# Performance work log

Measured on AMD Instinct MI355X. Metric: run time of the kernel, lower is better.

The kernel has to match this reference:

```python
import jax, jax.numpy as jnp
import numpy as np

# --- fixed physical constants (module params are requires_grad=False) ---
G = 9.81
M = 0.1667
CAF = 5.0 * 0.25 * M * G          # tanh(0) -> ratio = 1.0 exactly
CAR = CAF
LF = 0.09 - 0.036
LR = 0.036
IZ = 0.000267                      # tanh(0) -> pow_ratio = 0 -> Iz_base
THROTTLE_OFFSET = 0.24
THROTTLE_RATIO = 6.98
DT = 0.01
RES_BOUNDS = jnp.array([0.05 * G, 0.05 * G, 0.05 * G * 0.2], dtype=jnp.float32)

B, H, T = 131072, 4, 32


def setup_inputs() -> dict:
    key = jax.random.key(0)
    ks = jax.random.split(key, 8)
    # realistic car states: [x, vx_w, y, vy_w, psi, yaw_rate]
    pos = jax.random.normal(ks[0], (B, H, 2)) * 1.0
    vx = 2.0 + 0.2 * jax.random.normal(ks[1], (B, H, 1))
    vy = 0.1 * jax.random.normal(ks[2], (B, H, 1))
    psi = 0.2 * jax.random.normal(ks[3], (B, H, 1))
    r = 0.1 * jax.random.normal(ks[4], (B, H, 1))
    thr = 0.30 + 0.05 * jax.random.normal(ks[5], (B, H, 1))
    steer = 0.05 * jax.random.normal(ks[6], (B, H, 1))
    full_states = jnp.concatenate(
        [pos[..., :1], vx, pos[..., 1:], vy, psi, r, thr, steer], axis=-1
    ).astype(jnp.float32)
    ka = jax.random.split(ks[7], 6)
    actions = jnp.concatenate(
        [0.30 + 0.05 * jax.random.normal(ka[0], (B, T, 1)),
         0.05 * jax.random.normal(ka[1], (B, T, 1))], axis=-1).astype(jnp.float32)
    in_dim = H * 8
    fc1_w = (jax.random.normal(ka[2], (16, in_dim)) / np.sqrt(in_dim)).astype(jnp.float32)
    fc1_b = (0.01 * jax.random.normal(ka[3], (16,))).astype(jnp.float32)
    fc2_w = (jax.random.normal(ka[4], (3, 16)) / np.sqrt(16)).astype(jnp.float32)
    fc2_b = (0.01 * jax.random.normal(ka[5], (3,))).astype(jnp.float32)
    return {"full_states": full_states, "actions": actions,
            "fc1_w": fc1_w, "fc1_b": fc1_b, "fc2_w": fc2_w, "fc2_b": fc2_b,
            "enable_rnn": 1}


def _rollout(full_states, actions, fc1_w, fc1_b, fc2_w, fc2_b, enable_rnn):
    bsz = full_states.shape[0]
    a33 = lambda Vx: -(2 * CAF + 2 * CAR) / (M * Vx)
    a35 = lambda Vx: -Vx - (2 * CAF * LF - 2 * CAR * LR) / (M * Vx)
    a53 = lambda Vx: -(2 * LF * CAF - 2 * LR * CAR) / (IZ * Vx)
    a55 = lambda Vx: -(2 * LF ** 2 * CAF + 2 * LR ** 2 * CAR) / (IZ * Vx)

    def step(window, act):  # window [B,H,8], act [B,2]
        s = window[:, -1, :6]
        thr, steer = window[:, -1, 6], window[:, -1, 7]
        psi = s[:, 4]
        c, sn = jnp.cos(psi), jnp.sin(psi)
        Vx = s[:, 1] * c + s[:, 3] * sn
        # v = R(-psi) @ s  (body frame)
        v1 = c * s[:, 1] + sn * s[:, 3]
        v3 = -sn * s[:, 1] + c * s[:, 3]
        v5 = s[:, 5]
        long_acc = (thr - THROTTLE_OFFSET) * THROTTLE_RATIO
        # d = A @ v + B @ u
        d0 = v1
        d1 = long_acc
        d2 = v3
        d3 = a33(Vx) * v3 + a35(Vx) * v5 + (2 * CAF / M) * steer
        d4 = v5
        d5 = a53(Vx) * v3 + a55(Vx) * v5 + (2 * LF * CAF / IZ) * steer
        if enable_rnn:
            flat = window.reshape(bsz, -1)
            y1 = jnp.tanh(flat @ fc1_w.T + fc1_b)
            y2 = jnp.tanh(y1 @ fc2_w.T + fc2_b) * RES_BOUNDS[None, :]
            d1 = d1 + y2[:, 0] / M
            d3 = d3 + y2[:, 1] / M
            d5 = d5 + y2[:, 2] / IZ
        # s_new = s + R(psi) @ d * dt
        ns0 = s[:, 0] + (c * d0 - sn * d2) * DT
        ns1 = s[:, 1] + (c * d1 - sn * d3) * DT
        ns2 = s[:, 2] + (sn * d0 + c * d2) * DT
        ns3 = s[:, 3] + (sn * d1 + c * d3) * DT
        ns4 = jnp.mod(s[:, 4] + d4 * DT + jnp.pi, 2 * jnp.pi) - jnp.pi
        ns5 = s[:, 5] + d5 * DT
        new_full = jnp.stack([ns0, ns1, ns2, ns3, ns4, ns5, act[:, 0], act[:, 1]], axis=1)
        new_window = jnp.concatenate([window[:, 1:], new_full[:, None, :]], axis=1)
        return new_window, new_full

    acts_t = jnp.swapaxes(actions, 0, 1)  # [T,B,2]
    _, outs = jax.lax.scan(step, full_states, acts_t)
    return jnp.swapaxes(outs, 0, 1)  # [B,T,8]


def reference(full_states, actions, fc1_w, fc1_b, fc2_w, fc2_b, enable_rnn):
    return _rollout(full_states, actions, fc1_w, fc1_b, fc2_w, fc2_b, bool(enable_rnn))
```

## Files before the change

### kernel.cpp

```cpp
#include <hip/hip_runtime.h>
#include <math.h>

namespace {

typedef short  bf16x8 __attribute__((ext_vector_type(8)));
typedef float  f32x4  __attribute__((ext_vector_type(4)));

constexpr int B_TOTAL = 131072;
constexpr int T_STEPS = 32;

constexpr double dG   = 9.81;
constexpr double dM   = 0.1667;
constexpr double dCAF = 5.0 * 0.25 * dM * dG;
constexpr double dCAR = dCAF;
constexpr double dLF  = 0.09 - 0.036;
constexpr double dLR  = 0.036;
constexpr double dIZ  = 0.000267;

constexpr float A33N = (float)(-(2.0 * dCAF + 2.0 * dCAR));
constexpr float A35N = (float)(-(2.0 * dCAF * dLF - 2.0 * dCAR * dLR));
constexpr float A53N = (float)(-(2.0 * dLF * dCAF - 2.0 * dLR * dCAR));
constexpr float A55N = (float)(-(2.0 * dLF * dLF * dCAF + 2.0 * dLR * dLR * dCAR));
constexpr float ST1  = (float)(2.0 * dCAF / dM);
constexpr float ST5  = (float)(2.0 * dLF * dCAF / dIZ);
constexpr float MF   = (float)dM;
constexpr float IZF  = (float)dIZ;
constexpr float R0M  = (float)(0.05 * dG / dM);
constexpr float R1M  = (float)(0.05 * dG / dM);
constexpr float R2I  = (float)(0.05 * dG * 0.2 / dIZ);
constexpr float THR_OFF = 0.24f;
constexpr float THR_RAT = 6.98f;
constexpr float DT    = 0.01f;
constexpr float PI_F  = (float)3.14159265358979323846;
constexpr float TWOPI = (float)(2.0 * 3.14159265358979323846);
constexpr float INV2PI = (float)(1.0 / (2.0 * 3.14159265358979323846));
constexpr float TWO_LOG2E = 2.8853900817779268f;

__device__ __forceinline__ float fast_tanh(float x) {
    const float e = __builtin_amdgcn_exp2f(x * TWO_LOG2E);
    return fmaf(-2.0f, __builtin_amdgcn_rcpf(e + 1.0f), 1.0f);
}

__device__ __forceinline__ unsigned bf16_rne_u(float f) {
    unsigned u = __float_as_uint(f);
    return (u + 0x7fffu + ((u >> 16) & 1u)) >> 16;
}

__device__ __forceinline__ unsigned pk_bf16(float lo, float hi) {
    unsigned r;
    asm("v_cvt_pk_bf16_f32 %0, %1, %2" : "=v"(r) : "v"(lo), "v"(hi));
    return r;
}
__device__ __forceinline__ float bfl(unsigned p) { return __uint_as_float(p << 16); }
__device__ __forceinline__ float bfh(unsigned p) { return __uint_as_float(p & 0xffff0000u); }

union U4F { uint4 u; bf16x8 f; };

__global__ void prep_kernel(const float* __restrict__ w1, unsigned* __restrict__ ws) {
    const int i = threadIdx.x;
    if (i >= 256) return;
    const int p = i >> 6, L = i & 63;
    const int row = L & 15, g = L >> 4;
    const int pos = (g - p) & 3;
    unsigned hd[4], md[4], ld[4];
    #pragma unroll
    for (int d = 0; d < 4; ++d) {
        unsigned hh[2], mm[2], ll[2];
        #pragma unroll
        for (int s = 0; s < 2; ++s) {
            const float v = w1[row * 32 + pos * 8 + 2 * d + s];
            const unsigned h = bf16_rne_u(v);
            const float r1 = v - __uint_as_float(h << 16);
            const unsigned m = bf16_rne_u(r1);
            const float r2 = r1 - __uint_as_float(m << 16);
            const unsigned l = bf16_rne_u(r2);
            hh[s] = h; mm[s] = m; ll[s] = l;
        }
        hd[d] = hh[0] | (hh[1] << 16);
        md[d] = mm[0] | (mm[1] << 16);
        ld[d] = ll[0] | (ll[1] << 16);
    }
    uint4* w4 = reinterpret_cast<uint4*>(ws);
    w4[(p * 3 + 0) * 64 + L] = make_uint4(hd[0], hd[1], hd[2], hd[3]);
    w4[(p * 3 + 1) * 64 + L] = make_uint4(md[0], md[1], md[2], md[3]);
    w4[(p * 3 + 2) * 64 + L] = make_uint4(ld[0], ld[1], ld[2], ld[3]);
}

__device__ __forceinline__ int xbase(int e) { return (e * 64) ^ ((e & 7) << 4); }

__device__ __forceinline__ void split3_store(
    char* X, int off,
    float v0, float v1, float v2, float v3, float v4, float v5, float v6, float v7)
{
    const unsigned h0 = pk_bf16(v0, v1), h1 = pk_bf16(v2, v3);
    const unsigned h2 = pk_bf16(v4, v5), h3 = pk_bf16(v6, v7);
    const float r0 = v0 - bfl(h0), r1 = v1 - bfh(h0);
    const float r2 = v2 - bfl(h1), r3 = v3 - bfh(h1);
    const float r4 = v4 - bfl(h2), r5 = v5 - bfh(h2);
    const float r6 = v6 - bfl(h3), r7 = v7 - bfh(h3);
    const unsigned m0 = pk_bf16(r0, r1), m1 = pk_bf16(r2, r3);
    const unsigned m2 = pk_bf16(r4, r5), m3 = pk_bf16(r6, r7);
    const unsigned l0 = pk_bf16(r0 - bfl(m0), r1 - bfh(m0));
    const unsigned l1 = pk_bf16(r2 - bfl(m1), r3 - bfh(m1));
    const unsigned l2 = pk_bf16(r4 - bfl(m2), r5 - bfh(m2));
    const unsigned l3 = pk_bf16(r6 - bfl(m3), r7 - bfh(m3));
    *reinterpret_cast<uint4*>(X + off)        = make_uint4(h0, h1, h2, h3);
    *reinterpret_cast<uint4*>(X + 4096 + off) = make_uint4(m0, m1, m2, m3);
    *reinterpret_cast<uint4*>(X + 8192 + off) = make_uint4(l0, l1, l2, l3);
}

__global__ __launch_bounds__(64, 2)
void rollout_kernel(const float* __restrict__ fs,
                    const float* __restrict__ acts,
                    const unsigned* __restrict__ ws,
                    const float* __restrict__ b1g,
                    const float* __restrict__ w2g,
                    const float* __restrict__ b2g,
                    const int*   __restrict__ en,
                    float*       __restrict__ out)
{
    __shared__ char  X[12288];
    __shared__ float abuf[64 * 8];
    __shared__ float sbuf[64 * 16];

    const int L = threadIdx.x;
    const int g = L >> 4;
    const size_t blk = (size_t)blockIdx.x * 64;

    const int rnn = *en;

    bf16x8 Ah[4], Am[4], Al[4];
    {
        const uint4* w4 = reinterpret_cast<const uint4*>(ws);
        #pragma unroll
        for (int p = 0; p < 4; ++p) {
            U4F a; a.u = w4[(p * 3 + 0) * 64 + L]; Ah[p] = a.f;
            U4F b; b.u = w4[(p * 3 + 1) * 64 + L]; Am[p] = b.f;
            U4F c; c.u = w4[(p * 3 + 2) * 64 + L]; Al[p] = c.f;
        }
    }
    float b1s[4];
    #pragma unroll
    for (int r = 0; r < 4; ++r) b1s[r] = b1g[g * 4 + r];
    float w2s[3][4];
    #pragma unroll
    for (int c = 0; c < 3; ++c)
        #pragma unroll
        for (int r = 0; r < 4; ++r) w2s[c][r] = w2g[c * 16 + g * 4 + r];
    const float bias2_0 = b2g[0], bias2_1 = b2g[1], bias2_2 = b2g[2];

    int roffv[4];
    #pragma unroll
    for (int n = 0; n < 4; ++n) roffv[n] = xbase(16 * n + (L & 15)) ^ (g * 16);
    const int wboff = xbase(L);

    float s0, s1, s2, s3, s4, s5, thr, steer;
    {
        const float4* ip = reinterpret_cast<const float4*>(fs + (blk + L) * 32);
        #pragma unroll
        for (int rr = 0; rr < 4; ++rr) {
            const float4 va = ip[rr * 2], vb = ip[rr * 2 + 1];
            split3_store(X, wboff ^ (rr * 16), va.x, va.y, va.z, va.w, vb.x, vb.y, vb.z, vb.w);
            if (rr == 3) {
                s0 = va.x; s1 = va.y; s2 = va.z; s3 = va.w;
                s4 = vb.x; s5 = vb.y; thr = vb.z; steer = vb.w;
            }
        }
    }

    const f32x4 zero4 = {0.f, 0.f, 0.f, 0.f};
    const bool bb0 = (g & 1) != 0, bb1 = (g & 2) != 0;

    for (int tc = 0; tc < T_STEPS; tc += 4) {
        #pragma unroll
        for (int k = 0; k < 2; ++k) {
            const int q   = k * 64 + L;
            const int row = q >> 1;
            const int f4  = q & 1;
            const float4 v = *reinterpret_cast<const float4*>(
                &acts[(blk + row) * 64 + tc * 2 + f4 * 4]);
            *reinterpret_cast<float4*>(&abuf[row * 8 + ((f4 * 4) ^ (row & 4))]) = v;
        }

        #pragma unroll
        for (int tl = 0; tl < 4; ++tl) {
            const float2 act = *reinterpret_cast<const float2*>(
                &abuf[L * 8 + ((2 * tl) ^ (L & 4))]);
            const float ax = act.x, ay = act.y;

            const float rev = s4 * INV2PI;
            const float sn = __builtin_amdgcn_sinf(rev);
            const float c  = __builtin_amdgcn_cosf(rev);

            const float Vx = s1 * c + s3 * sn;
            const float v3 = c * s3 - sn * s1;
            const float v5 = s5;

            const float inv_mvx  = __builtin_amdgcn_rcpf(MF * Vx);
            const float inv_izvx = __builtin_amdgcn_rcpf(IZF * Vx);
            const float a33 = A33N * inv_mvx;
            const float a35 = -Vx + A35N * inv_mvx;
            const float a53 = A53N * inv_izvx;
            const float a55 = A55N * inv_izvx;

            const float d0 = Vx;
            float       d1 = (thr - THR_OFF) * THR_RAT;
            const float d2 = v3;
            float       d3 = a33 * v3 + a35 * v5 + ST1 * steer;
            const float d4 = v5;
            float       d5 = a53 * v3 + a55 * v5 + ST5 * steer;

            if (rnn) {
                f32x4 acc[4];
                #pragma unroll
                for (int n = 0; n < 4; ++n) {
                    U4F bh; bh.u = *reinterpret_cast<const uint4*>(X + roffv[n]);
                    U4F bm; bm.u = *reinterpret_cast<const uint4*>(X + 4096 + roffv[n]);
                    U4F bl; bl.u = *reinterpret_cast<const uint4*>(X + 8192 + roffv[n]);
                    f32x4 a = __builtin_amdgcn_mfma_f32_16x16x32_bf16(Ah[tl], bl.f, zero4, 0, 0, 0);
                    a = __builtin_amdgcn_mfma_f32_16x16x32_bf16(Al[tl], bh.f, a, 0, 0, 0);
                    a = __builtin_amdgcn_mfma_f32_16x16x32_bf16(Am[tl], bm.f, a, 0, 0, 0);
                    a = __builtin_amdgcn_mfma_f32_16x16x32_bf16(Am[tl], bh.f, a, 0, 0, 0);
                    a = __builtin_amdgcn_mfma_f32_16x16x32_bf16(Ah[tl], bm.f, a, 0, 0, 0);
                    acc[n] = __builtin_amdgcn_mfma_f32_16x16x32_bf16(Ah[tl], bh.f, a, 0, 0, 0);
                }
                float p0[4], p1[4], p2[4];
                #pragma unroll
                for (int n = 0; n < 4; ++n) {
                    float q0 = 0.f, q1 = 0.f, q2 = 0.f;
                    #pragma unroll
                    for (int r = 0; r < 4; ++r) {
                        const float y = fast_tanh(acc[n][r] + b1s[r]);
                        q0 = fmaf(w2s[0][r], y, q0);
                        q1 = fmaf(w2s[1][r], y, q1);
                        q2 = fmaf(w2s[2][r], y, q2);
                    }
                    p0[n] = q0; p1[n] = q1; p2[n] = q2;
                }
                float z0, z1, z2;
                #pragma unroll
                for (int c3 = 0; c3 < 3; ++c3) {
                    const float* p = (c3 == 0) ? p0 : (c3 == 1) ? p1 : p2;
                    const float own = bb1 ? (bb0 ? p[3] : p[2]) : (bb0 ? p[1] : p[0]);
                    const float x1  = bb1 ? (bb0 ? p[2] : p[3]) : (bb0 ? p[0] : p[1]);
                    const float x2  = bb1 ? (bb0 ? p[1] : p[0]) : (bb0 ? p[3] : p[2]);
                    const float x3  = bb1 ? (bb0 ? p[0] : p[1]) : (bb0 ? p[2] : p[3]);
                    const float a = own + __shfl_xor(x1, 16, 64);
                    const float b = x2  + __shfl_xor(x3, 16, 64);
                    const float T = a + __shfl_xor(b, 32, 64);
                    if (c3 == 0) z0 = T; else if (c3 == 1) z1 = T; else z2 = T;
                }
                d1 += fast_tanh(z0 + bias2_0) * R0M;
                d3 += fast_tanh(z1 + bias2_1) * R1M;
                d5 += fast_tanh(z2 + bias2_2) * R2I;
            }

            const float ns0 = s0 + (c * d0 - sn * d2) * DT;
            const float ns1 = s1 + (c * d1 - sn * d3) * DT;
            const float ns2 = s2 + (sn * d0 + c * d2) * DT;
            const float ns3 = s3 + (sn * d1 + c * d3) * DT;
            float aa = s4 + d4 * DT + PI_F;
            aa = aa - floorf(aa * INV2PI) * TWOPI;
            const float ns4 = aa - PI_F;
            const float ns5 = s5 + d5 * DT;

            const int c4b = (tl & 1) * 2;
            *reinterpret_cast<float4*>(&sbuf[L * 16 + 4 * ((c4b + 0) ^ (L & 3))]) =
                make_float4(ns0, ns1, ns2, ns3);
            *reinterpret_cast<float4*>(&sbuf[L * 16 + 4 * ((c4b + 1) ^ (L & 3))]) =
                make_float4(ns4, ns5, ax, ay);

            if (rnn) {
                split3_store(X, wboff ^ (tl * 16), ns0, ns1, ns2, ns3, ns4, ns5, ax, ay);
            }

            s0 = ns0; s1 = ns1; s2 = ns2; s3 = ns3;
            s4 = ns4; s5 = ns5; thr = ax; steer = ay;

            if (tl & 1) {
                const int t2 = tc + tl - 1;
                #pragma unroll
                for (int k = 0; k < 4; ++k) {
                    const int q   = k * 64 + L;
                    const int row = q >> 2;
                    const int f   = q & 3;
                    const float4 v = *reinterpret_cast<const float4*>(
                        &sbuf[row * 16 + 4 * (f ^ (row & 3))]);
                    *reinterpret_cast<float4*>(&out[(blk + row) * 256 + t2 * 8 + f * 4]) = v;
                }
            }
        }
    }
}

}

extern "C" void kernel_launch(void* const* d_in, const int* in_sizes, int n_in,
                              void* d_out, int out_size, void* d_ws, size_t ws_size,
                              hipStream_t stream) {
    const float* fs = (const float*)d_in[0];
    const float* ac = (const float*)d_in[1];
    const float* w1 = (const float*)d_in[2];
    const float* b1 = (const float*)d_in[3];
    const float* w2 = (const float*)d_in[4];
    const float* b2 = (const float*)d_in[5];
    const int*   en = (const int*)d_in[6];
    float* out = (float*)d_out;
    unsigned* ws = (unsigned*)d_ws;

    hipLaunchKernelGGL(prep_kernel, dim3(1), dim3(256), 0, stream, w1, ws);

    dim3 grid(B_TOTAL / 64), block(64);
    hipLaunchKernelGGL(rollout_kernel, grid, block, 0, stream,
                       fs, ac, ws, b1, w2, b2, en, out);
}
```

Baseline: 74.37 us.

## Process two batch chunks per wave and prefetch next action chunk

Each 64-lane wave now handles 128 elements as two independent chains, so the MFMA/tanh work of one chunk can interleave with the other and hide dependency latency. LDS buffers double and launch bounds drop to one block per SIMD hint. Action loads for the next 4-step chunk are issued early into registers to overlap global latency. The cost is higher register and LDS use, which may lower occupancy, and half as many blocks.

```diff
diff --git a/kernel.cpp b/kernel.cpp
--- a/kernel.cpp
+++ b/kernel.cpp
@@ -8,6 +8,7 @@
 
 constexpr int B_TOTAL = 131072;
 constexpr int T_STEPS = 32;
+constexpr int EPW     = 128;
 
 constexpr double dG   = 9.81;
 constexpr double dM   = 0.1667;
@@ -104,12 +105,12 @@
     const unsigned l1 = pk_bf16(r2 - bfl(m1), r3 - bfh(m1));
     const unsigned l2 = pk_bf16(r4 - bfl(m2), r5 - bfh(m2));
     const unsigned l3 = pk_bf16(r6 - bfl(m3), r7 - bfh(m3));
-    *reinterpret_cast<uint4*>(X + off)        = make_uint4(h0, h1, h2, h3);
-    *reinterpret_cast<uint4*>(X + 4096 + off) = make_uint4(m0, m1, m2, m3);
-    *reinterpret_cast<uint4*>(X + 8192 + off) = make_uint4(l0, l1, l2, l3);
-}
-
-__global__ __launch_bounds__(64, 2)
+    *reinterpret_cast<uint4*>(X + off)         = make_uint4(h0, h1, h2, h3);
+    *reinterpret_cast<uint4*>(X + 8192 + off)  = make_uint4(m0, m1, m2, m3);
+    *reinterpret_cast<uint4*>(X + 16384 + off) = make_uint4(l0, l1, l2, l3);
+}
+
+__global__ __launch_bounds__(64, 1)
 void rollout_kernel(const float* __restrict__ fs,
                     const float* __restrict__ acts,
                     const unsigned* __restrict__ ws,
@@ -119,13 +120,13 @@
                     const int*   __restrict__ en,
                     float*       __restrict__ out)
 {
-    __shared__ char  X[12288];
-    __shared__ float abuf[64 * 8];
-    __shared__ float sbuf[64 * 16];
+    __shared__ char  X[24576];
+    __shared__ float abuf[EPW * 8];
+    __shared__ float sbuf[EPW * 16];
 
     const int L = threadIdx.x;
     const int g = L >> 4;
-    const size_t blk = (size_t)blockIdx.x * 64;
+    const size_t blk = (size_t)blockIdx.x * EPW;
 
     const int rnn = *en;
 
@@ -149,138 +150,176 @@
         for (int r = 0; r < 4; ++r) w2s[c][r] = w2g[c * 16 + g * 4 + r];
     const float bias2_0 = b2g[0], bias2_1 = b2g[1], bias2_2 = b2g[2];
 
-    int roffv[4];
-    #pragma unroll
-    for (int n = 0; n < 4; ++n) roffv[n] = xbase(16 * n + (L & 15)) ^ (g * 16);
-    const int wboff = xbase(L);
-
-    float s0, s1, s2, s3, s4, s5, thr, steer;
-    {
-        const float4* ip = reinterpret_cast<const float4*>(fs + (blk + L) * 32);
+    int roffv[8];
+    #pragma unroll
+    for (int n = 0; n < 8; ++n) roffv[n] = xbase(16 * n + (L & 15)) ^ (g * 16);
+    int wboff[2];
+    wboff[0] = xbase(L);
+    wboff[1] = xbase(64 + L);
+
+    int ar[4], aw[4];
+    #pragma unroll
+    for (int k = 0; k < 4; ++k) {
+        ar[k] = k * 32 + (L >> 1);
+        aw[k] = ar[k] * 8 + (((L & 1) * 4) ^ (ar[k] & 4));
+    }
+
+    float S0[2], S1[2], S2[2], S3[2], S4[2], S5[2], TH[2], SR[2];
+    #pragma unroll
+    for (int ch = 0; ch < 2; ++ch) {
+        const int e = ch * 64 + L;
+        const float4* ip = reinterpret_cast<const float4*>(fs + (blk + e) * 32);
         #pragma unroll
         for (int rr = 0; rr < 4; ++rr) {
             const float4 va = ip[rr * 2], vb = ip[rr * 2 + 1];
-            split3_store(X, wboff ^ (rr * 16), va.x, va.y, va.z, va.w, vb.x, vb.y, vb.z, vb.w);
+            split3_store(X, wboff[ch] ^ (rr * 16), va.x, va.y, va.z, va.w, vb.x, vb.y, vb.z, vb.w);
             if (rr == 3) {
-                s0 = va.x; s1 = va.y; s2 = va.z; s3 = va.w;
-                s4 = vb.x; s5 = vb.y; thr = vb.z; steer = vb.w;
+                S0[ch] = va.x; S1[ch] = va.y; S2[ch] = va.z; S3[ch] = va.w;
+                S4[ch] = vb.x; S5[ch] = vb.y; TH[ch] = vb.z; SR[ch] = vb.w;
             }
         }
     }
+
+    float4 ga0 = *reinterpret_cast<const float4*>(&acts[(blk + ar[0]) * 64 + (L & 1) * 4]);
+    float4 ga1 = *reinterpret_cast<const float4*>(&acts[(blk + ar[1]) * 64 + (L & 1) * 4]);
+    float4 ga2 = *reinterpret_cast<const float4*>(&acts[(blk + ar[2]) * 64 + (L & 1) * 4]);
+    float4 ga3 = *reinterpret_cast<const float4*>(&acts[(blk + ar[3]) * 64 + (L & 1) * 4]);
 
     const f32x4 zero4 = {0.f, 0.f, 0.f, 0.f};
     const bool bb0 = (g & 1) != 0, bb1 = (g & 2) != 0;
 
     for (int tc = 0; tc < T_STEPS; tc += 4) {
-        #pragma unroll
-        for (int k = 0; k < 2; ++k) {
-            const int q   = k * 64 + L;
-            const int row = q >> 1;
-            const int f4  = q & 1;
-            const float4 v = *reinterpret_cast<const float4*>(
-                &acts[(blk + row) * 64 + tc * 2 + f4 * 4]);
-            *reinterpret_cast<float4*>(&abuf[row * 8 + ((f4 * 4) ^ (row & 4))]) = v;
+        *reinterpret_cast<float4*>(&abuf[aw[0]]) = ga0;
+        *reinterpret_cast<float4*>(&abuf[aw[1]]) = ga1;
+        *reinterpret_cast<float4*>(&abuf[aw[2]]) = ga2;
+        *reinterpret_cast<float4*>(&abuf[aw[3]]) = ga3;
+        float4 av0[2], av1[2];
+        #pragma unroll
+        for (int ch = 0; ch < 2; ++ch) {
+            const int e = ch * 64 + L;
+            av0[ch] = *reinterpret_cast<const float4*>(&abuf[e * 8 + (0 ^ (L & 4))]);
+            av1[ch] = *reinterpret_cast<const float4*>(&abuf[e * 8 + (4 ^ (L & 4))]);
+        }
+        if (tc + 4 < T_STEPS) {
+            ga0 = *reinterpret_cast<const float4*>(&acts[(blk + ar[0]) * 64 + (tc + 4) * 2 + (L & 1) * 4]);
+            ga1 = *reinterpret_cast<const float4*>(&acts[(blk + ar[1]) * 64 + (tc + 4) * 2 + (L & 1) * 4]);
+            ga2 = *reinterpret_cast<const float4*>(&acts[(blk + ar[2]) * 64 + (tc + 4) * 2 + (L & 1) * 4]);
+            ga3 = *reinterpret_cast<const float4*>(&acts[(blk + ar[3]) * 64 + (tc + 4) * 2 + (L & 1) * 4]);
         }
 
         #pragma unroll
         for (int tl = 0; tl < 4; ++tl) {
-            const float2 act = *reinterpret_cast<const float2*>(
-                &abuf[L * 8 + ((2 * tl) ^ (L & 4))]);
-            const float ax = act.x, ay = act.y;
-
-            const float rev = s4 * INV2PI;
-            const float sn = __builtin_amdgcn_sinf(rev);
-            const float c  = __builtin_amdgcn_cosf(rev);
-
-            const float Vx = s1 * c + s3 * sn;
-            const float v3 = c * s3 - sn * s1;
-            const float v5 = s5;
-
-            const float inv_mvx  = __builtin_amdgcn_rcpf(MF * Vx);
-            const float inv_izvx = __builtin_amdgcn_rcpf(IZF * Vx);
-            const float a33 = A33N * inv_mvx;
-            const float a35 = -Vx + A35N * inv_mvx;
-            const float a53 = A53N * inv_izvx;
-            const float a55 = A55N * inv_izvx;
-
-            const float d0 = Vx;
-            float       d1 = (thr - THR_OFF) * THR_RAT;
-            const float d2 = v3;
-            float       d3 = a33 * v3 + a35 * v5 + ST1 * steer;
-            const float d4 = v5;
-            float       d5 = a53 * v3 + a55 * v5 + ST5 * steer;
+            float AX[2], AY[2];
+            float Z0[2], Z1[2], Z2[2];
 
             if (rnn) {
-                f32x4 acc[4];
                 #pragma unroll
-                for (int n = 0; n < 4; ++n) {
-                    U4F bh; bh.u = *reinterpret_cast<const uint4*>(X + roffv[n]);
-                    U4F bm; bm.u = *reinterpret_cast<const uint4*>(X + 4096 + roffv[n]);
-                    U4F bl; bl.u = *reinterpret_cast<const uint4*>(X + 8192 + roffv[n]);
-                    f32x4 a = __builtin_amdgcn_mfma_f32_16x16x32_bf16(Ah[tl], bl.f, zero4, 0, 0, 0);
-                    a = __builtin_amdgcn_mfma_f32_16x16x32_bf16(Al[tl], bh.f, a, 0, 0, 0);
-                    a = __builtin_amdgcn_mfma_f32_16x16x32_bf16(Am[tl], bm.f, a, 0, 0, 0);
-                    a = __builtin_amdgcn_mfma_f32_16x16x32_bf16(Am[tl], bh.f, a, 0, 0, 0);
-                    a = __builtin_amdgcn_mfma_f32_16x16x32_bf16(Ah[tl], bm.f, a, 0, 0, 0);
-                    acc[n] = __builtin_amdgcn_mfma_f32_16x16x32_bf16(Ah[tl], bh.f, a, 0, 0, 0);
+                for (int ch = 0; ch < 2; ++ch) {
+                    f32x4 acc[4];
+                    #pragma unroll
+                    for (int n = 0; n < 4; ++n) {
+                        const int ro = roffv[ch * 4 + n];
+                        U4F bh; bh.u = *reinterpret_cast<const uint4*>(X + ro);
+                        U4F bm; bm.u = *reinterpret_cast<const uint4*>(X + 8192 + ro);
+                        U4F bl; bl.u = *reinterpret_cast<const uint4*>(X + 16384 + ro);
+                        f32x4 a = __builtin_amdgcn_mfma_f32_16x16x32_bf16(Ah[tl], bl.f, zero4, 0, 0, 0);
+                        a = __builtin_amdgcn_mfma_f32_16x16x32_bf16(Al[tl], bh.f, a, 0, 0, 0);
+                        a = __builtin_amdgcn_mfma_f32_16x16x32_bf16(Am[tl], bm.f, a, 0, 0, 0);
+                        a = __builtin_amdgcn_mfma_f32_16x16x32_bf16(Am[tl], bh.f, a, 0, 0, 0);
+                        a = __builtin_amdgcn_mfma_f32_16x16x32_bf16(Ah[tl], bm.f, a, 0, 0, 0);
+                        acc[n] = __builtin_amdgcn_mfma_f32_16x16x32_bf16(Ah[tl], bh.f, a, 0, 0, 0);
+                    }
+                    float p0[4], p1[4], p2[4];
+                    #pragma unroll
+                    for (int n = 0; n < 4; ++n) {
+                        float q0 = 0.f, q1 = 0.f, q2 = 0.f;
+                        #pragma unroll
+                        for (int r = 0; r < 4; ++r) {
+                            const float y = fast_tanh(acc[n][r] + b1s[r]);
+                            q0 = fmaf(w2s[0][r], y, q0);
+                            q1 = fmaf(w2s[1][r], y, q1);
+                            q2 = fmaf(w2s[2][r], y, q2);
+                        }
+                        p0[n] = q0; p1[n] = q1; p2[n] = q2;
+                    }
+                    #pragma unroll
+                    for (int c3 = 0; c3 < 3; ++c3) {
+                        const float* p = (c3 == 0) ? p0 : (c3 == 1) ? p1 : p2;
+                        const float own = bb1 ? (bb0 ? p[3] : p[2]) : (bb0 ? p[1] : p[0]);
+                        const float x1  = bb1 ? (bb0 ? p[2] : p[3]) : (bb0 ? p[0] : p[1]);
+                        const float x2  = bb1 ? (bb0 ? p[1] : p[0]) : (bb0 ? p[3] : p[2]);
+                        const float x3  = bb1 ? (bb0 ? p[0] : p[1]) : (bb0 ? p[2] : p[3]);
+                        const float a = own + __shfl_xor(x1, 16, 64);
+                        const float b = x2  + __shfl_xor(x3, 16, 64);
+                        const float T = a + __shfl_xor(b, 32, 64);
+                        if (c3 == 0) Z0[ch] = T; else if (c3 == 1) Z1[ch] = T; else Z2[ch] = T;
+                    }
                 }
-                float p0[4], p1[4], p2[4];
-                #pragma unroll
-                for (int n = 0; n < 4; ++n) {
-                    float q0 = 0.f, q1 = 0.f, q2 = 0.f;
-                    #pragma unroll
-                    for (int r = 0; r < 4; ++r) {
-                        const float y = fast_tanh(acc[n][r] + b1s[r]);
-                        q0 = fmaf(w2s[0][r], y, q0);
-                        q1 = fmaf(w2s[1][r], y, q1);
-                        q2 = fmaf(w2s[2][r], y, q2);
-                    }
-                    p0[n] = q0; p1[n] = q1; p2[n] = q2;
+            }
+
+            #pragma unroll
+            for (int ch = 0; ch < 2; ++ch) {
+                const float4 a01 = av0[ch], a23 = av1[ch];
+                const float ax = (tl == 0) ? a01.x : (tl == 1) ? a01.z : (tl == 2) ? a23.x : a23.z;
+                const float ay = (tl == 0) ? a01.y : (tl == 1) ? a01.w : (tl == 2) ? a23.y : a23.w;
+                AX[ch] = ax; AY[ch] = ay;
+
+                const float rev = S4[ch] * INV2PI;
+                const float sn = __builtin_amdgcn_sinf(rev);
+                const float c  = __builtin_amdgcn_cosf(rev);
+
+                const float Vx = S1[ch] * c + S3[ch] * sn;
+                const float v3 = c * S3[ch] - sn * S1[ch];
+                const float v5 = S5[ch];
+
+                const float inv_mvx  = __builtin_amdgcn_rcpf(MF * Vx);
+                const float inv_izvx = __builtin_amdgcn_rcpf(IZF * Vx);
+                const float a33 = A33N * inv_mvx;
+                const float a35 = -Vx + A35N * inv_mvx;
+                const float a53 = A53N * inv_izvx;
+                const float a55 = A55N * inv_izvx;
+
+                const float d0 = Vx;
+                float       d1 = (TH[ch] - THR_OFF) * THR_RAT;
+                const float d2 = v3;
+                float       d3 = a33 * v3 + a35 * v5 + ST1 * SR[ch];
+                const float d4 = v5;
+                float       d5 = a53 * v3 + a55 * v5 + ST5 * SR[ch];
+
+                if (rnn) {
+                    d1 += fast_tanh(Z0[ch] + bias2_0) * R0M;
+                    d3 += fast_tanh(Z1[ch] + bias2_1) * R1M;
+                    d5 += fast_tanh(Z2[ch] + bias2_2) * R2I;
                 }
-                float z0, z1, z2;
-                #pragma unroll
-                for (int c3 = 0; c3 < 3; ++c3) {
-                    const float* p = (c3 == 0) ? p0 : (c3 == 1) ? p1 : p2;
-                    const float own = bb1 ? (bb0 ? p[3] : p[2]) : (bb0 ? p[1] : p[0]);
-                    const float x1  = bb1 ? (bb0 ? p[2] : p[3]) : (bb0 ? p[0] : p[1]);
-                    const float x2  = bb1 ? (bb0 ? p[1] : p[0]) : (bb0 ? p[3] : p[2]);
-                    const float x3  = bb1 ? (bb0 ? p[0] : p[1]) : (bb0 ? p[2] : p[3]);
-                    const float a = own + __shfl_xor(x1, 16, 64);
-                    const float b = x2  + __shfl_xor(x3, 16, 64);
-                    const float T = a + __shfl_xor(b, 32, 64);
-                    if (c3 == 0) z0 = T; else if (c3 == 1) z1 = T; else z2 = T;
+
+                const float ns0 = S0[ch] + (c * d0 - sn * d2) * DT;
+                const float ns1 = S1[ch] + (c * d1 - sn * d3) * DT;
+                const float ns2 = S2[ch] + (sn * d0 + c * d2) * DT;
+                const float ns3 = S3[ch] + (sn * d1 + c * d3) * DT;
+                float aa = S4[ch] + d4 * DT + PI_F;
+                aa = aa - floorf(aa * INV2PI) * TWOPI;
+                const float ns4 = aa - PI_F;
+                const float ns5 = S5[ch] + d5 * DT;
+
+                const int e = ch * 64 + L;
+                const int c4b = (tl & 1) * 2;
+                *reinterpret_cast<float4*>(&sbuf[e * 16 + 4 * ((c4b + 0) ^ (L & 3))]) =
+                    make_float4(ns0, ns1, ns2, ns3);
+                *reinterpret_cast<float4*>(&sbuf[e * 16 + 4 * ((c4b + 1) ^ (L & 3))]) =
+                    make_float4(ns4, ns5, ax, ay);
+
+                if (rnn) {
+                    split3_store(X, wboff[ch] ^ (tl * 16), ns0, ns1, ns2, ns3, ns4, ns5, ax, ay);
                 }
-                d1 += fast_tanh(z0 + bias2_0) * R0M;
-                d3 += fast_tanh(z1 + bias2_1) * R1M;
-                d5 += fast_tanh(z2 + bias2_2) * R2I;
+
+                S0[ch] = ns0; S1[ch] = ns1; S2[ch] = ns2; S3[ch] = ns3;
+                S4[ch] = ns4; S5[ch] = ns5; TH[ch] = ax;  SR[ch] = ay;
             }
-
-            const float ns0 = s0 + (c * d0 - sn * d2) * DT;
-            const float ns1 = s1 + (c * d1 - sn * d3) * DT;
-            const float ns2 = s2 + (sn * d0 + c * d2) * DT;
-            const float ns3 = s3 + (sn * d1 + c * d3) * DT;
-            float aa = s4 + d4 * DT + PI_F;
-            aa = aa - floorf(aa * INV2PI) * TWOPI;
-            const float ns4 = aa - PI_F;
-            const float ns5 = s5 + d5 * DT;
-
-            const int c4b = (tl & 1) * 2;
-            *reinterpret_cast<float4*>(&sbuf[L * 16 + 4 * ((c4b + 0) ^ (L & 3))]) =
-                make_float4(ns0, ns1, ns2, ns3);
-            *reinterpret_cast<float4*>(&sbuf[L * 16 + 4 * ((c4b + 1) ^ (L & 3))]) =
-                make_float4(ns4, ns5, ax, ay);
-
-            if (rnn) {
-                split3_store(X, wboff ^ (tl * 16), ns0, ns1, ns2, ns3, ns4, ns5, ax, ay);
-            }
-
-            s0 = ns0; s1 = ns1; s2 = ns2; s3 = ns3;
-            s4 = ns4; s5 = ns5; thr = ax; steer = ay;
 
             if (tl & 1) {
                 const int t2 = tc + tl - 1;
                 #pragma unroll
-                for (int k = 0; k < 4; ++k) {
+                for (int k = 0; k < 8; ++k) {
                     const int q   = k * 64 + L;
                     const int row = q >> 2;
                     const int f   = q & 3;
@@ -310,7 +349,7 @@
 
     hipLaunchKernelGGL(prep_kernel, dim3(1), dim3(256), 0, stream, w1, ws);
 
-    dim3 grid(B_TOTAL / 64), block(64);
+    dim3 grid(B_TOTAL / EPW), block(64);
     hipLaunchKernelGGL(rollout_kernel, grid, block, 0, stream,
                        fs, ac, ws, b1, w2, b2, en, out);
 }
```

Result: slower. 84.82 us (+14.0%).
